# Optimization experiments

Hardware: AMD Instinct MI355X
Metric: run time of the kernel (lower is better)

The kernel has to match this reference:

```python
import jax, jax.numpy as jnp
import numpy as np

N, E, NF, EF = 2048, 65536, 128, 64
HID, NH, HD, FF, L = 256, 8, 32, 1024, 4
OUT, MAXN = 1280, 4096


def setup_inputs() -> dict:
    key = jax.random.key(0)
    ks = iter(jax.random.split(key, 64))
    def rn(shape, s=0.02):
        return jax.random.normal(next(ks), shape, jnp.float32) * s
    inp = dict(
        node_features=jax.random.normal(next(ks), (N, NF), jnp.float32),
        edge_features=jax.random.normal(next(ks), (E, EF), jnp.float32),
        edge_index=jax.random.randint(next(ks), (2, E), 0, N),
        W_node=rn((NF, HID)), b_node=jnp.zeros((HID,)),
        W_edge=rn((EF, HID)), b_edge=jnp.zeros((HID,)),
        pos_emb=rn((MAXN, HID), 1.0),
        Wq=rn((L, HID, HID)), bq=jnp.zeros((L, HID)),
        Wk=rn((L, HID, HID)), bk=jnp.zeros((L, HID)),
        Wv=rn((L, HID, HID)), bv=jnp.zeros((L, HID)),
        Wo=rn((L, HID, HID)), bo=jnp.zeros((L, HID)),
        Wep=rn((L, HID, NH)), bep=jnp.zeros((L, NH)),
        Wf1=rn((L, HID, FF)), bf1=jnp.zeros((L, FF)),
        Wf2=rn((L, FF, HID)), bf2=jnp.zeros((L, HID)),
        g1=jnp.ones((L, HID)), be1=jnp.zeros((L, HID)),
        g2=jnp.ones((L, HID)), be2=jnp.zeros((L, HID)),
        g_ln=jnp.ones((HID,)), b_ln=jnp.zeros((HID,)),
        Wp1=rn((HID, HID)), bp1=jnp.zeros((HID,)),
        Wp2=rn((HID, 1)), bp2=jnp.zeros((1,)),
        Wo1=rn((3 * HID, 2 * HID)), bo1=jnp.zeros((2 * HID,)),
        Wo2=rn((2 * HID, OUT)), bo2=jnp.zeros((OUT,)),
    )
    return inp


def _ln(x, g, b, eps=1e-5):
    m = x.mean(-1, keepdims=True)
    v = ((x - m) ** 2).mean(-1, keepdims=True)
    return (x - m) * jax.lax.rsqrt(v + eps) * g + b


def reference(node_features, edge_features, edge_index, W_node, b_node, W_edge,
              b_edge, pos_emb, Wq, bq, Wk, bk, Wv, bv, Wo, bo, Wep, bep,
              Wf1, bf1, Wf2, bf2, g1, be1, g2, be2, g_ln, b_ln,
              Wp1, bp1, Wp2, bp2, Wo1, bo1, Wo2, bo2):
    n = node_features.shape[0]
    src, dst = edge_index[0], edge_index[1]
    scale = float(np.sqrt(HD))
    # node encoding + learned positional embedding (n <= max_nodes path)
    x = node_features @ W_node + b_node + pos_emb[:n]
    edge_attr = edge_features @ W_edge + b_edge  # [E, HID]
    # symmetric adjacency mask with self-loops
    adj = jnp.zeros((n, n), bool).at[src, dst].set(True).at[dst, src].set(True)
    adj = adj.at[jnp.arange(n), jnp.arange(n)].set(True)
    for i in range(L):
        Q = (x @ Wq[i] + bq[i]).reshape(n, NH, HD)
        K = (x @ Wk[i] + bk[i]).reshape(n, NH, HD)
        V = (x @ Wv[i] + bv[i]).reshape(n, NH, HD)
        scores = jnp.einsum('nhd,mhd->nmh', Q, K) / scale  # [n, n, NH]
        ebias = edge_attr @ Wep[i] + bep[i]  # [E, NH]
        scores = scores.at[src, dst].add(ebias)  # accumulating scatter, same as per-edge loop
        scores = jnp.where(adj[:, None, :], scores.transpose(0, 2, 1), -jnp.inf)  # [n, NH, n]
        attn = jax.nn.softmax(scores, axis=-1)
        ctx = jnp.einsum('nhm,mhd->nhd', attn, V).reshape(n, HID)
        a = ctx @ Wo[i] + bo[i]
        x = _ln(x + a, g1[i], be1[i])
        f = jax.nn.gelu(x @ Wf1[i] + bf1[i], approximate=False) @ Wf2[i] + bf2[i]
        x = _ln(x + f, g2[i], be2[i])
    x = _ln(x, g_ln, b_ln)
    # global pooling (batch=None path): mean / max / attention
    mean_p = x.mean(0, keepdims=True)
    max_p = x.max(0, keepdims=True)
    aw = jax.nn.softmax(jnp.tanh(x @ Wp1 + bp1) @ Wp2 + bp2, axis=0)  # [n, 1]
    attn_p = (x * aw).sum(0, keepdims=True)
    g = jnp.concatenate([mean_p, max_p, attn_p], axis=1)  # [1, 3*HID]
    out = jax.nn.relu(g @ Wo1 + bo1) @ Wo2 + bo2  # [1, OUT]
    return out
```

## Files before the change

kernel.cpp:

```cpp
#include <hip/hip_runtime.h>
#include <math.h>

#define NNODE 2048
#define NEDGE 65536
#define HIDN  256
#define NHEAD 8
#define HDIM  32
#define FFD   1024
#define NLAYER 4
#define OUTD  1280
#define NNZ_MAX (2*NEDGE + NNODE)

typedef __attribute__((ext_vector_type(8))) short bf16x8;
typedef __attribute__((ext_vector_type(4))) float f32x4;

__device__ __forceinline__ unsigned short f2b(float f) {
    unsigned u = __float_as_uint(f);
    unsigned r = (u + 0x7fffu + ((u >> 16) & 1u)) >> 16;
    return (unsigned short)r;
}
__device__ __forceinline__ float b2f(unsigned short u) {
    return __uint_as_float((unsigned)u << 16);
}

template<int EPI, int OUT>
__global__ __launch_bounds__(256)
void mgemm(const unsigned short* __restrict__ A, const unsigned short* __restrict__ Bt,
           const float* __restrict__ bias, const float* __restrict__ extra,
           float* __restrict__ Cf, unsigned short* __restrict__ Cb,
           int M, int N, int K)
{
    __shared__ __align__(16) unsigned short As[64 * 40];
    __shared__ __align__(16) unsigned short Bs[64 * 40];
    int tid = threadIdx.x;
    int bm0 = blockIdx.y * 64, bn0 = blockIdx.x * 64;
    int wave = tid >> 6, lane = tid & 63;
    int wm = (wave >> 1) * 32, wn = (wave & 1) * 32;
    int srow = tid >> 2, skoff = (tid & 3) * 8;
    int lrow = lane & 15, quad = lane >> 4;
    f32x4 acc[2][2] = {};
    for (int k0 = 0; k0 < K; k0 += 32) {
        *(uint4*)(&As[srow*40 + skoff]) = *(const uint4*)(A  + (size_t)(bm0+srow)*K + k0 + skoff);
        *(uint4*)(&Bs[srow*40 + skoff]) = *(const uint4*)(Bt + (size_t)(bn0+srow)*K + k0 + skoff);
        __syncthreads();
        bf16x8 af[2], bfr[2];
        #pragma unroll
        for (int i = 0; i < 2; i++) af[i]  = *(const bf16x8*)(&As[(wm + i*16 + lrow)*40 + quad*8]);
        #pragma unroll
        for (int j = 0; j < 2; j++) bfr[j] = *(const bf16x8*)(&Bs[(wn + j*16 + lrow)*40 + quad*8]);
        #pragma unroll
        for (int i = 0; i < 2; i++)
            #pragma unroll
            for (int j = 0; j < 2; j++)
                acc[i][j] = __builtin_amdgcn_mfma_f32_16x16x32_bf16(af[i], bfr[j], acc[i][j], 0, 0, 0);
        __syncthreads();
    }
    #pragma unroll
    for (int i = 0; i < 2; i++)
        #pragma unroll
        for (int j = 0; j < 2; j++) {
            int col = bn0 + wn + j*16 + lrow;
            float bv = bias[col];
            #pragma unroll
            for (int r = 0; r < 4; r++) {
                int row = bm0 + wm + i*16 + quad*4 + r;
                float v = acc[i][j][r] + bv;
                if (EPI == 1) v = 0.5f * v * (1.f + erff(v * 0.70710678118654752f));
                else if (EPI == 2) v = tanhf(v);
                else if (EPI == 3) v += extra[(size_t)row*N + col];
                if (OUT == 0 || OUT == 2) Cf[(size_t)row*N + col] = v;
                if (OUT == 1 || OUT == 2) Cb[(size_t)row*N + col] = f2b(v);
            }
        }
}

__global__ __launch_bounds__(256)
void transpose_bf16(const float* __restrict__ src, unsigned short* __restrict__ dst,
                    int K, int N, long srcStride, long dstStride)
{
    __shared__ unsigned short tile[32][33];
    const float* s = src + (size_t)blockIdx.z * srcStride;
    unsigned short* d = dst + (size_t)blockIdx.z * dstStride;
    int n0 = blockIdx.x * 32, k0 = blockIdx.y * 32;
    int tx = threadIdx.x & 31, ty = threadIdx.x >> 5;
    #pragma unroll
    for (int i = 0; i < 4; i++)
        tile[ty + i*8][tx] = f2b(s[(size_t)(k0 + ty + i*8) * N + n0 + tx]);
    __syncthreads();
    #pragma unroll
    for (int i = 0; i < 4; i++)
        d[(size_t)(n0 + ty + i*8) * K + k0 + tx] = tile[tx][ty + i*8];
}

__global__ void conv_bf16(const float* __restrict__ s, unsigned short* __restrict__ d, int n)
{
    int t = blockIdx.x * 256 + threadIdx.x;
    if (t < n) d[t] = f2b(s[t]);
}

__global__ void concat_qkv_bias(const float* __restrict__ bq, const float* __restrict__ bk,
                                const float* __restrict__ bv, float* __restrict__ bqkv)
{
    int t = blockIdx.x * 256 + threadIdx.x;
    if (t >= NLAYER * 768) return;
    int l = t / 768, j = t % 768;
    float v = (j < 256) ? bq[l*256 + j] : (j < 512 ? bk[l*256 + j - 256] : bv[l*256 + j - 512]);
    bqkv[t] = v;
}

__global__ void adj_build(const int* __restrict__ src, const int* __restrict__ dst,
                          unsigned* __restrict__ adjbits)
{
    int t = blockIdx.x * blockDim.x + threadIdx.x;
    if (t < NEDGE) {
        int s = src[t], d = dst[t];
        atomicOr(&adjbits[(size_t)s*64 + (d >> 5)], 1u << (d & 31));
        atomicOr(&adjbits[(size_t)d*64 + (s >> 5)], 1u << (s & 31));
    }
    if (t < NNODE)
        atomicOr(&adjbits[(size_t)t*64 + (t >> 5)], 1u << (t & 31));
}

__global__ void row_rank(const unsigned* __restrict__ adjbits,
                         unsigned* __restrict__ rowcum, int* __restrict__ deg)
{
    int i = blockIdx.x * blockDim.x + threadIdx.x;
    if (i >= NNODE) return;
    unsigned c = 0;
    for (int w = 0; w < 64; w++) {
        rowcum[i*64 + w] = c;
        c += __popc(adjbits[i*64 + w]);
    }
    deg[i] = (int)c;
}

__global__ __launch_bounds__(256)
void scan_kernel(const int* __restrict__ deg, int* __restrict__ rowoff)
{
    __shared__ int part[256];
    int tid = threadIdx.x;
    int base = tid * 8;
    int local[8]; int s = 0;
    #pragma unroll
    for (int k = 0; k < 8; k++) { local[k] = s; s += deg[base + k]; }
    part[tid] = s;
    __syncthreads();
    for (int off = 1; off < 256; off <<= 1) {
        int v = (tid >= off) ? part[tid - off] : 0;
        __syncthreads();
        part[tid] += v;
        __syncthreads();
    }
    int pre = (tid == 0) ? 0 : part[tid - 1];
    #pragma unroll
    for (int k = 0; k < 8; k++) rowoff[base + k] = pre + local[k];
    if (tid == 255) rowoff[NNODE] = part[255];
}

__global__ void fill_cols(const unsigned* __restrict__ adjbits,
                          const int* __restrict__ rowoff, int* __restrict__ cols)
{
    int i = blockIdx.x * blockDim.x + threadIdx.x;
    if (i >= NNODE) return;
    int base = rowoff[i];
    for (int w = 0; w < 64; w++) {
        unsigned bits = adjbits[i*64 + w];
        while (bits) {
            int b = __ffs(bits) - 1;
            cols[base++] = w*32 + b;
            bits &= bits - 1;
        }
    }
}

__global__ void wcomb_kernel(const float* __restrict__ W_edge, const float* __restrict__ b_edge,
                             const float* __restrict__ Wep, const float* __restrict__ bep,
                             float* __restrict__ Wcomb, float* __restrict__ bcomb)
{
    int t = blockIdx.x * blockDim.x + threadIdx.x;
    if (t < 64*32) {
        int k = t >> 5, lh = t & 31, l = lh >> 3, h = lh & 7;
        float acc = 0.f;
        for (int c = 0; c < HIDN; c++)
            acc += W_edge[k*HIDN + c] * Wep[l*HIDN*NHEAD + c*NHEAD + h];
        Wcomb[k*32 + lh] = acc;
    } else if (t < 64*32 + 32) {
        int lh = t - 64*32, l = lh >> 3, h = lh & 7;
        float acc = bep[l*NHEAD + h];
        for (int c = 0; c < HIDN; c++)
            acc += b_edge[c] * Wep[l*HIDN*NHEAD + c*NHEAD + h];
        bcomb[lh] = acc;
    }
}

__global__ __launch_bounds__(256)
void ebias_kernel(const float* __restrict__ ef, const float* __restrict__ Wcomb,
                  const float* __restrict__ bcomb, float* __restrict__ out)
{
    __shared__ float Wl[64*32];
    __shared__ float bl[32];
    int tid = threadIdx.x;
    for (int k = tid; k < 64*32; k += 256) Wl[k] = Wcomb[k];
    if (tid < 32) bl[tid] = bcomb[tid];
    __syncthreads();
    int t = blockIdx.x * 256 + tid;
    int e = t >> 5, lh = t & 31;
    const float* f = ef + (size_t)e * 64;
    float acc = bl[lh];
    #pragma unroll
    for (int k = 0; k < 64; k++) acc += f[k] * Wl[k*32 + lh];
    out[(size_t)e*32 + lh] = acc;
}

__global__ void scatter_bias(const int* __restrict__ src, const int* __restrict__ dst,
                             const unsigned* __restrict__ adjbits,
                             const unsigned* __restrict__ rowcum,
                             const int* __restrict__ rowoff,
                             const float* __restrict__ ebias, float* __restrict__ bias_csr)
{
    int t = blockIdx.x * blockDim.x + threadIdx.x;
    int e = t >> 5;
    if (e >= NEDGE) return;
    int lh = t & 31;
    int s = src[e], d = dst[e];
    unsigned wbits = adjbits[(size_t)s*64 + (d >> 5)];
    int rank = (int)rowcum[(size_t)s*64 + (d >> 5)] + __popc(wbits & ((1u << (d & 31)) - 1u));
    int slot = rowoff[s] + rank;
    atomicAdd(&bias_csr[(size_t)slot*32 + lh], ebias[(size_t)e*32 + lh]);
}

__global__ __launch_bounds__(256)
void attn_kernel(const unsigned short* __restrict__ QKVb, const int* __restrict__ rowoff,
                 const int* __restrict__ cols, const float* __restrict__ bias_csr,
                 unsigned short* __restrict__ ctxb, int layer)
{
    __shared__ float mS[4][8], lS[4][8];
    __shared__ __align__(16) float accS[4][256];
    int i = blockIdx.x;
    int tid = threadIdx.x;
    int w = tid >> 6, lane = tid & 63;
    int h = lane >> 3;
    int off = lane * 4;
    ushort4 qu = *(const ushort4*)(QKVb + (size_t)i*768 + off);
    float4 qf = { b2f(qu.x), b2f(qu.y), b2f(qu.z), b2f(qu.w) };
    int start = rowoff[i], end = rowoff[i+1];
    int lh0 = layer * 8 + h;
    float m = -INFINITY, l = 0.f;
    float4 acc = {0.f, 0.f, 0.f, 0.f};
    for (int c0 = start + w; c0 < end; c0 += 256) {
        int myslot = c0 + 4*lane;
        int mycol = (myslot < end) ? cols[myslot] : 0;
        int lim = min(end, c0 + 256);
        int it = 0;
        for (int slot = c0; slot < lim; slot += 4, ++it) {
            int j = __shfl(mycol, it);
            ushort4 ku = *(const ushort4*)(QKVb + (size_t)j*768 + 256 + off);
            float s = qf.x*b2f(ku.x) + qf.y*b2f(ku.y) + qf.z*b2f(ku.z) + qf.w*b2f(ku.w);
            s += __shfl_xor(s, 1);
            s += __shfl_xor(s, 2);
            s += __shfl_xor(s, 4);
            s = s * 0.17677669529663687f + bias_csr[(size_t)slot*32 + lh0];
            float mn = fmaxf(m, s);
            float sc = __expf(m - mn);
            float p  = __expf(s - mn);
            ushort4 vu = *(const ushort4*)(QKVb + (size_t)j*768 + 512 + off);
            acc.x = acc.x*sc + p*b2f(vu.x);
            acc.y = acc.y*sc + p*b2f(vu.y);
            acc.z = acc.z*sc + p*b2f(vu.z);
            acc.w = acc.w*sc + p*b2f(vu.w);
            l = l*sc + p;
            m = mn;
        }
    }
    if ((lane & 7) == 0) { mS[w][h] = m; lS[w][h] = l; }
    *(float4*)&accS[w][off] = acc;
    __syncthreads();
    if (w == 0) {
        float m0 = mS[0][h], m1 = mS[1][h], m2 = mS[2][h], m3 = mS[3][h];
        float mx = fmaxf(fmaxf(m0, m1), fmaxf(m2, m3));
        float e0 = (m0 == -INFINITY) ? 0.f : __expf(m0 - mx);
        float e1 = (m1 == -INFINITY) ? 0.f : __expf(m1 - mx);
        float e2 = (m2 == -INFINITY) ? 0.f : __expf(m2 - mx);
        float e3 = (m3 == -INFINITY) ? 0.f : __expf(m3 - mx);
        float ls = lS[0][h]*e0 + lS[1][h]*e1 + lS[2][h]*e2 + lS[3][h]*e3;
        float4 a0 = *(float4*)&accS[0][off];
        float4 a1 = *(float4*)&accS[1][off];
        float4 a2 = *(float4*)&accS[2][off];
        float4 a3 = *(float4*)&accS[3][off];
        float inv = 1.f / ls;
        ushort4 o;
        o.x = f2b((a0.x*e0 + a1.x*e1 + a2.x*e2 + a3.x*e3) * inv);
        o.y = f2b((a0.y*e0 + a1.y*e1 + a2.y*e2 + a3.y*e3) * inv);
        o.z = f2b((a0.z*e0 + a1.z*e1 + a2.z*e2 + a3.z*e3) * inv);
        o.w = f2b((a0.w*e0 + a1.w*e1 + a2.w*e2 + a3.w*e3) * inv);
        *(ushort4*)(ctxb + (size_t)i*HIDN + off) = o;
    }
}

template<bool RES>
__global__ __launch_bounds__(256)
void ln_kernel(float* __restrict__ x, const float* __restrict__ r,
               const float* __restrict__ g, const float* __restrict__ b,
               unsigned short* __restrict__ xb)
{
    __shared__ float lds[4];
    int row = blockIdx.x, c = threadIdx.x;
    float v = x[(size_t)row*HIDN + c];
    if (RES) v += r[(size_t)row*HIDN + c];
    float s = v;
    for (int mm = 1; mm < 64; mm <<= 1) s += __shfl_xor(s, mm);
    if ((c & 63) == 0) lds[c >> 6] = s;
    __syncthreads();
    float mean = (lds[0] + lds[1] + lds[2] + lds[3]) * (1.f / HIDN);
    __syncthreads();
    float dv = v - mean;
    float qq = dv * dv;
    for (int mm = 1; mm < 64; mm <<= 1) qq += __shfl_xor(qq, mm);
    if ((c & 63) == 0) lds[c >> 6] = qq;
    __syncthreads();
    float var = (lds[0] + lds[1] + lds[2] + lds[3]) * (1.f / HIDN);
    float rs = rsqrtf(var + 1e-5f);
    float o = dv * rs * g[c] + b[c];
    x[(size_t)row*HIDN + c] = o;
    xb[(size_t)row*HIDN + c] = f2b(o);
}

__global__ void pool_score(const float* __restrict__ t, const float* __restrict__ Wp2,
                           const float* __restrict__ bp2, float* __restrict__ s)
{
    int i = blockIdx.x * blockDim.x + threadIdx.x;
    if (i >= NNODE) return;
    float acc = bp2[0];
    for (int c = 0; c < HIDN; c++) acc += t[(size_t)i*HIDN + c] * Wp2[c];
    s[i] = acc;
}

__global__ __launch_bounds__(1024)
void softmax_nodes(const float* __restrict__ s, float* __restrict__ aw)
{
    __shared__ float lds[16];
    __shared__ float red;
    int tid = threadIdx.x;
    float a = s[tid], b = s[tid + 1024];
    float mx = fmaxf(a, b);
    for (int mm = 1; mm < 64; mm <<= 1) mx = fmaxf(mx, __shfl_xor(mx, mm));
    if ((tid & 63) == 0) lds[tid >> 6] = mx;
    __syncthreads();
    if (tid == 0) { float v = -INFINITY; for (int k = 0; k < 16; k++) v = fmaxf(v, lds[k]); red = v; }
    __syncthreads();
    mx = red;
    float ea = __expf(a - mx), eb = __expf(b - mx);
    float ss = ea + eb;
    for (int mm = 1; mm < 64; mm <<= 1) ss += __shfl_xor(ss, mm);
    __syncthreads();
    if ((tid & 63) == 0) lds[tid >> 6] = ss;
    __syncthreads();
    if (tid == 0) { float v = 0.f; for (int k = 0; k < 16; k++) v += lds[k]; red = v; }
    __syncthreads();
    ss = red;
    aw[tid] = ea / ss;
    aw[tid + 1024] = eb / ss;
}

__global__ __launch_bounds__(256)
void pool_kernel(const float* __restrict__ x, const float* __restrict__ aw,
                 float* __restrict__ g)
{
    __shared__ float l1[4], l2[4], l3[4];
    int c = blockIdx.x, tid = threadIdx.x;
    float sm = 0.f, mx = -INFINITY, ap = 0.f;
    for (int r = tid; r < NNODE; r += 256) {
        float v = x[(size_t)r*HIDN + c];
        sm += v;
        mx = fmaxf(mx, v);
        ap += v * aw[r];
    }
    for (int mm = 1; mm < 64; mm <<= 1) {
        sm += __shfl_xor(sm, mm);
        mx = fmaxf(mx, __shfl_xor(mx, mm));
        ap += __shfl_xor(ap, mm);
    }
    if ((tid & 63) == 0) { int w = tid >> 6; l1[w] = sm; l2[w] = mx; l3[w] = ap; }
    __syncthreads();
    if (tid == 0) {
        sm = l1[0] + l1[1] + l1[2] + l1[3];
        mx = fmaxf(fmaxf(l2[0], l2[1]), fmaxf(l2[2], l2[3]));
        ap = l3[0] + l3[1] + l3[2] + l3[3];
        g[c]          = sm * (1.f / NNODE);
        g[HIDN + c]   = mx;
        g[2*HIDN + c] = ap;
    }
}

__global__ __launch_bounds__(512)
void head1(const float* __restrict__ g, const float* __restrict__ Wo1,
           const float* __restrict__ bo1, float* __restrict__ h1)
{
    __shared__ float gs[3*HIDN];
    int tid = threadIdx.x;
    for (int k = tid; k < 3*HIDN; k += 512) gs[k] = g[k];
    __syncthreads();
    float acc = bo1[tid];
    for (int k = 0; k < 3*HIDN; k++) acc += gs[k] * Wo1[(size_t)k*512 + tid];
    h1[tid] = fmaxf(acc, 0.f);
}

__global__ __launch_bounds__(256)
void head2(const float* __restrict__ h1, const float* __restrict__ Wo2,
           const float* __restrict__ bo2, float* __restrict__ out)
{
    __shared__ float hs[512];
    int tid = threadIdx.x;
    int j = blockIdx.x * 256 + tid;
    for (int k = tid; k < 512; k += 256) hs[k] = h1[k];
    __syncthreads();
    float acc = bo2[j];
    for (int k = 0; k < 512; k++) acc += hs[k] * Wo2[(size_t)k*OUTD + j];
    out[j] = acc;
}

extern "C" void kernel_launch(void* const* d_in, const int* in_sizes, int n_in,
                              void* d_out, int out_size, void* d_ws, size_t ws_size,
                              hipStream_t stream)
{
    const float* node_features = (const float*)d_in[0];
    const float* edge_features = (const float*)d_in[1];
    const int*   edge_index    = (const int*)d_in[2];
    const float* W_node = (const float*)d_in[3];
    const float* b_node = (const float*)d_in[4];
    const float* W_edge = (const float*)d_in[5];
    const float* b_edge = (const float*)d_in[6];
    const float* pos_emb = (const float*)d_in[7];
    const float* Wq = (const float*)d_in[8];
    const float* bq = (const float*)d_in[9];
    const float* Wk = (const float*)d_in[10];
    const float* bk = (const float*)d_in[11];
    const float* Wv = (const float*)d_in[12];
    const float* bv = (const float*)d_in[13];
    const float* Wo = (const float*)d_in[14];
    const float* bo = (const float*)d_in[15];
    const float* Wep = (const float*)d_in[16];
    const float* bep = (const float*)d_in[17];
    const float* Wf1 = (const float*)d_in[18];
    const float* bf1 = (const float*)d_in[19];
    const float* Wf2 = (const float*)d_in[20];
    const float* bf2 = (const float*)d_in[21];
    const float* g1  = (const float*)d_in[22];
    const float* be1 = (const float*)d_in[23];
    const float* g2  = (const float*)d_in[24];
    const float* be2 = (const float*)d_in[25];
    const float* g_ln = (const float*)d_in[26];
    const float* b_ln = (const float*)d_in[27];
    const float* Wp1 = (const float*)d_in[28];
    const float* bp1 = (const float*)d_in[29];
    const float* Wp2 = (const float*)d_in[30];
    const float* bp2 = (const float*)d_in[31];
    const float* Wo1 = (const float*)d_in[32];
    const float* bo1 = (const float*)d_in[33];
    const float* Wo2 = (const float*)d_in[34];
    const float* bo2 = (const float*)d_in[35];
    const int* src = edge_index;
    const int* dst = edge_index + NEDGE;

    char* w = (char*)d_ws;
    auto carve = [&](size_t nbytes) {
        void* p = (void*)w;
        w += (nbytes + 255) & ~(size_t)255;
        return p;
    };
    float* x        = (float*)carve((size_t)NNODE*HIDN*4);
    unsigned short* xb = (unsigned short*)carve((size_t)NNODE*HIDN*2);
    unsigned short* bufQKVb = (unsigned short*)carve((size_t)NNODE*768*2);
    float* bufO     = (float*)carve((size_t)NNODE*HIDN*4);
    float* bufP     = (float*)carve((size_t)NNODE*HIDN*4);
    unsigned short* bufAb = (unsigned short*)carve((size_t)NNODE*HIDN*2);
    void*  scratchA = carve((size_t)NEDGE*32*4);
    float* bufE     = (float*)scratchA;
    unsigned short* bufFb = (unsigned short*)scratchA;
    float* Wcomb    = (float*)carve(64*32*4);
    float* bcomb    = (float*)carve(32*4);
    unsigned* adjbits = (unsigned*)carve((size_t)NNODE*64*4);
    unsigned* rowcum  = (unsigned*)carve((size_t)NNODE*64*4);
    int* deg    = (int*)carve(NNODE*4);
    int* rowoff = (int*)carve((NNODE+1)*4);
    int* colsb  = (int*)carve((size_t)NNZ_MAX*4);
    float* bias_csr = (float*)carve((size_t)NNZ_MAX*32*4);
    float* sbuf  = (float*)carve(NNODE*4);
    float* awbuf = (float*)carve(NNODE*4);
    float* gbuf  = (float*)carve(3*HIDN*4);
    float* h1buf = (float*)carve(512*4);
    unsigned short* nf_b  = (unsigned short*)carve((size_t)NNODE*128*2);
    unsigned short* WnT   = (unsigned short*)carve((size_t)HIDN*128*2);
    unsigned short* WqkvT = (unsigned short*)carve((size_t)NLAYER*768*HIDN*2);
    float*          bqkv  = (float*)carve((size_t)NLAYER*768*4);
    unsigned short* WoT   = (unsigned short*)carve((size_t)NLAYER*HIDN*HIDN*2);
    unsigned short* Wf1T  = (unsigned short*)carve((size_t)NLAYER*FFD*HIDN*2);
    unsigned short* Wf2T  = (unsigned short*)carve((size_t)NLAYER*HIDN*FFD*2);
    unsigned short* Wp1T  = (unsigned short*)carve((size_t)HIDN*HIDN*2);

    hipMemsetAsync(adjbits, 0, (size_t)NNODE*64*4, stream);
    hipMemsetAsync(bias_csr, 0, (size_t)NNZ_MAX*32*4, stream);
    adj_build<<<(NEDGE+255)/256, 256, 0, stream>>>(src, dst, adjbits);
    row_rank<<<NNODE/256, 256, 0, stream>>>(adjbits, rowcum, deg);
    scan_kernel<<<1, 256, 0, stream>>>(deg, rowoff);
    fill_cols<<<NNODE/256, 256, 0, stream>>>(adjbits, rowoff, colsb);
    wcomb_kernel<<<(64*32+32+255)/256, 256, 0, stream>>>(W_edge, b_edge, Wep, bep, Wcomb, bcomb);
    ebias_kernel<<<(NEDGE*32)/256, 256, 0, stream>>>(edge_features, Wcomb, bcomb, bufE);
    scatter_bias<<<(NEDGE*32)/256, 256, 0, stream>>>(src, dst, adjbits, rowcum, rowoff, bufE, bias_csr);

    conv_bf16<<<(NNODE*128)/256, 256, 0, stream>>>(node_features, nf_b, NNODE*128);
    transpose_bf16<<<dim3(HIDN/32, 128/32, 1), 256, 0, stream>>>(W_node, WnT, 128, HIDN, 0, 0);
    transpose_bf16<<<dim3(8, 8, NLAYER), 256, 0, stream>>>(Wq, WqkvT,            HIDN, HIDN, 65536, 196608);
    transpose_bf16<<<dim3(8, 8, NLAYER), 256, 0, stream>>>(Wk, WqkvT + 65536,    HIDN, HIDN, 65536, 196608);
    transpose_bf16<<<dim3(8, 8, NLAYER), 256, 0, stream>>>(Wv, WqkvT + 131072,   HIDN, HIDN, 65536, 196608);
    transpose_bf16<<<dim3(8, 8, NLAYER), 256, 0, stream>>>(Wo, WoT, HIDN, HIDN, 65536, 65536);
    transpose_bf16<<<dim3(FFD/32, HIDN/32, NLAYER), 256, 0, stream>>>(Wf1, Wf1T, HIDN, FFD, 262144, 262144);
    transpose_bf16<<<dim3(HIDN/32, FFD/32, NLAYER), 256, 0, stream>>>(Wf2, Wf2T, FFD, HIDN, 262144, 262144);
    transpose_bf16<<<dim3(8, 8, 1), 256, 0, stream>>>(Wp1, Wp1T, HIDN, HIDN, 0, 0);
    concat_qkv_bias<<<(NLAYER*768+255)/256, 256, 0, stream>>>(bq, bk, bv, bqkv);

    mgemm<3,2><<<dim3(HIDN/64, NNODE/64), 256, 0, stream>>>(nf_b, WnT, b_node, pos_emb, x, xb, NNODE, HIDN, 128);

    for (int l = 0; l < NLAYER; l++) {
        mgemm<0,1><<<dim3(768/64, NNODE/64), 256, 0, stream>>>(
            xb, WqkvT + (size_t)l*768*HIDN, bqkv + l*768, nullptr, nullptr, bufQKVb, NNODE, 768, HIDN);
        attn_kernel<<<NNODE, 256, 0, stream>>>(bufQKVb, rowoff, colsb, bias_csr, bufAb, l);
        mgemm<0,0><<<dim3(HIDN/64, NNODE/64), 256, 0, stream>>>(
            bufAb, WoT + (size_t)l*HIDN*HIDN, bo + l*HIDN, nullptr, bufO, nullptr, NNODE, HIDN, HIDN);
        ln_kernel<true><<<NNODE, 256, 0, stream>>>(x, bufO, g1 + l*HIDN, be1 + l*HIDN, xb);
        mgemm<1,1><<<dim3(FFD/64, NNODE/64), 256, 0, stream>>>(
            xb, Wf1T + (size_t)l*FFD*HIDN, bf1 + l*FFD, nullptr, nullptr, bufFb, NNODE, FFD, HIDN);
        mgemm<0,0><<<dim3(HIDN/64, NNODE/64), 256, 0, stream>>>(
            bufFb, Wf2T + (size_t)l*HIDN*FFD, bf2 + l*HIDN, nullptr, bufO, nullptr, NNODE, HIDN, FFD);
        ln_kernel<true><<<NNODE, 256, 0, stream>>>(x, bufO, g2 + l*HIDN, be2 + l*HIDN, xb);
    }

    ln_kernel<false><<<NNODE, 256, 0, stream>>>(x, nullptr, g_ln, b_ln, xb);
    mgemm<2,0><<<dim3(HIDN/64, NNODE/64), 256, 0, stream>>>(xb, Wp1T, bp1, nullptr, bufP, nullptr, NNODE, HIDN, HIDN);
    pool_score<<<NNODE/256, 256, 0, stream>>>(bufP, Wp2, bp2, sbuf);
    softmax_nodes<<<1, 1024, 0, stream>>>(sbuf, awbuf);
    pool_kernel<<<HIDN, 256, 0, stream>>>(x, awbuf, gbuf);
    head1<<<1, 512, 0, stream>>>(gbuf, Wo1, bo1, h1buf);
    head2<<<OUTD/256, 256, 0, stream>>>(h1buf, Wo2, bo2, (float*)d_out);
}
```

Baseline: 554.9 us.

## Retile GEMM with large K chunks, fuse edge-bias scatter, parallelize fill_cols, merge launches

The GEMM now uses 32x64 output tiles and stages up to 256 K elements per shared-memory load, which cuts barriers and doubles the block count for the small-N GEMMs. The edge-bias projection is fused into the atomic scatter so the intermediate edge buffer is never written and read back. fill_cols becomes one thread per 32-bit word, using rowcum offsets, instead of one thread per row. The Q/K/V/O weight transposes are merged into a single launch, and the two memsets become one over adjacent buffers. The larger shared-memory footprint (about 50KB per block) may lower occupancy.

```diff
diff --git a/kernel.cpp b/kernel.cpp
--- a/kernel.cpp
+++ b/kernel.cpp
@@ -30,48 +30,53 @@
            float* __restrict__ Cf, unsigned short* __restrict__ Cb,
            int M, int N, int K)
 {
-    __shared__ __align__(16) unsigned short As[64 * 40];
-    __shared__ __align__(16) unsigned short Bs[64 * 40];
-    int tid = threadIdx.x;
-    int bm0 = blockIdx.y * 64, bn0 = blockIdx.x * 64;
+    __shared__ __align__(16) unsigned short As[32 * 264];
+    __shared__ __align__(16) unsigned short Bs[64 * 264];
+    int tid = threadIdx.x;
+    int bm0 = blockIdx.y * 32, bn0 = blockIdx.x * 64;
     int wave = tid >> 6, lane = tid & 63;
-    int wm = (wave >> 1) * 32, wn = (wave & 1) * 32;
-    int srow = tid >> 2, skoff = (tid & 3) * 8;
+    int wm = (wave & 1) * 16, wn = (wave >> 1) * 32;
     int lrow = lane & 15, quad = lane >> 4;
-    f32x4 acc[2][2] = {};
-    for (int k0 = 0; k0 < K; k0 += 32) {
-        *(uint4*)(&As[srow*40 + skoff]) = *(const uint4*)(A  + (size_t)(bm0+srow)*K + k0 + skoff);
-        *(uint4*)(&Bs[srow*40 + skoff]) = *(const uint4*)(Bt + (size_t)(bn0+srow)*K + k0 + skoff);
+    f32x4 acc[2] = {};
+    int kc = (K < 256) ? K : 256;
+    int ldl = kc + 8;
+    int upr = kc >> 3;
+    for (int k0 = 0; k0 < K; k0 += kc) {
+        int nA = 32 * upr;
+        for (int u = tid; u < nA; u += 256) {
+            int row = u / upr, col = (u % upr) * 8;
+            *(uint4*)(&As[row*ldl + col]) = *(const uint4*)(A + (size_t)(bm0+row)*K + k0 + col);
+        }
+        int nB = 64 * upr;
+        for (int u = tid; u < nB; u += 256) {
+            int row = u / upr, col = (u % upr) * 8;
+            *(uint4*)(&Bs[row*ldl + col]) = *(const uint4*)(Bt + (size_t)(bn0+row)*K + k0 + col);
+        }
         __syncthreads();
-        bf16x8 af[2], bfr[2];
+        for (int kk = 0; kk < kc; kk += 32) {
+            bf16x8 a  = *(const bf16x8*)(&As[(wm + lrow)*ldl + kk + quad*8]);
+            bf16x8 b0 = *(const bf16x8*)(&Bs[(wn + lrow)*ldl + kk + quad*8]);
+            bf16x8 b1 = *(const bf16x8*)(&Bs[(wn + 16 + lrow)*ldl + kk + quad*8]);
+            acc[0] = __builtin_amdgcn_mfma_f32_16x16x32_bf16(a, b0, acc[0], 0, 0, 0);
+            acc[1] = __builtin_amdgcn_mfma_f32_16x16x32_bf16(a, b1, acc[1], 0, 0, 0);
+        }
+        __syncthreads();
+    }
+    #pragma unroll
+    for (int j = 0; j < 2; j++) {
+        int col = bn0 + wn + j*16 + lrow;
+        float bv = bias[col];
         #pragma unroll
-        for (int i = 0; i < 2; i++) af[i]  = *(const bf16x8*)(&As[(wm + i*16 + lrow)*40 + quad*8]);
-        #pragma unroll
-        for (int j = 0; j < 2; j++) bfr[j] = *(const bf16x8*)(&Bs[(wn + j*16 + lrow)*40 + quad*8]);
-        #pragma unroll
-        for (int i = 0; i < 2; i++)
-            #pragma unroll
-            for (int j = 0; j < 2; j++)
-                acc[i][j] = __builtin_amdgcn_mfma_f32_16x16x32_bf16(af[i], bfr[j], acc[i][j], 0, 0, 0);
-        __syncthreads();
-    }
-    #pragma unroll
-    for (int i = 0; i < 2; i++)
-        #pragma unroll
-        for (int j = 0; j < 2; j++) {
-            int col = bn0 + wn + j*16 + lrow;
-            float bv = bias[col];
-            #pragma unroll
-            for (int r = 0; r < 4; r++) {
-                int row = bm0 + wm + i*16 + quad*4 + r;
-                float v = acc[i][j][r] + bv;
-                if (EPI == 1) v = 0.5f * v * (1.f + erff(v * 0.70710678118654752f));
-                else if (EPI == 2) v = tanhf(v);
-                else if (EPI == 3) v += extra[(size_t)row*N + col];
-                if (OUT == 0 || OUT == 2) Cf[(size_t)row*N + col] = v;
-                if (OUT == 1 || OUT == 2) Cb[(size_t)row*N + col] = f2b(v);
-            }
+        for (int r = 0; r < 4; r++) {
+            int row = bm0 + wm + quad*4 + r;
+            float v = acc[j][r] + bv;
+            if (EPI == 1) v = 0.5f * v * (1.f + erff(v * 0.70710678118654752f));
+            else if (EPI == 2) v = tanhf(v);
+            else if (EPI == 3) v += extra[(size_t)row*N + col];
+            if (OUT == 0 || OUT == 2) Cf[(size_t)row*N + col] = v;
+            if (OUT == 1 || OUT == 2) Cb[(size_t)row*N + col] = f2b(v);
         }
+    }
 }
 
 __global__ __launch_bounds__(256)
@@ -90,6 +95,28 @@
     #pragma unroll
     for (int i = 0; i < 4; i++)
         d[(size_t)(n0 + ty + i*8) * K + k0 + tx] = tile[tx][ty + i*8];
+}
+
+__global__ __launch_bounds__(256)
+void transpose_qkvo(const float* __restrict__ Wq, const float* __restrict__ Wk,
+                    const float* __restrict__ Wv, const float* __restrict__ Wo,
+                    unsigned short* __restrict__ WqkvT, unsigned short* __restrict__ WoT)
+{
+    __shared__ unsigned short tile[32][33];
+    int z = blockIdx.z;
+    int mat = z & 3, l = z >> 2;
+    const float* s = (mat == 0 ? Wq : mat == 1 ? Wk : mat == 2 ? Wv : Wo) + (size_t)l * 65536;
+    unsigned short* d = (mat < 3) ? WqkvT + (size_t)l*196608 + (size_t)mat*65536
+                                  : WoT + (size_t)l*65536;
+    int n0 = blockIdx.x * 32, k0 = blockIdx.y * 32;
+    int tx = threadIdx.x & 31, ty = threadIdx.x >> 5;
+    #pragma unroll
+    for (int i = 0; i < 4; i++)
+        tile[ty + i*8][tx] = f2b(s[(size_t)(k0 + ty + i*8) * 256 + n0 + tx]);
+    __syncthreads();
+    #pragma unroll
+    for (int i = 0; i < 4; i++)
+        d[(size_t)(n0 + ty + i*8) * 256 + k0 + tx] = tile[tx][ty + i*8];
 }
 
 __global__ void conv_bf16(const float* __restrict__ s, unsigned short* __restrict__ d, int n)
@@ -157,19 +184,18 @@
     if (tid == 255) rowoff[NNODE] = part[255];
 }
 
-__global__ void fill_cols(const unsigned* __restrict__ adjbits,
-                          const int* __restrict__ rowoff, int* __restrict__ cols)
-{
-    int i = blockIdx.x * blockDim.x + threadIdx.x;
-    if (i >= NNODE) return;
-    int base = rowoff[i];
-    for (int w = 0; w < 64; w++) {
-        unsigned bits = adjbits[i*64 + w];
-        while (bits) {
-            int b = __ffs(bits) - 1;
-            cols[base++] = w*32 + b;
-            bits &= bits - 1;
-        }
+__global__ __launch_bounds__(256)
+void fill_cols(const unsigned* __restrict__ adjbits, const int* __restrict__ rowoff,
+               const unsigned* __restrict__ rowcum, int* __restrict__ cols)
+{
+    int t = blockIdx.x * 256 + threadIdx.x;
+    int i = t >> 6, w = t & 63;
+    unsigned bits = adjbits[(size_t)i*64 + w];
+    int base = rowoff[i] + (int)rowcum[(size_t)i*64 + w];
+    while (bits) {
+        int b = __ffs(bits) - 1;
+        cols[base++] = w*32 + b;
+        bits &= bits - 1;
     }
 }
 
@@ -194,8 +220,12 @@
 }
 
 __global__ __launch_bounds__(256)
-void ebias_kernel(const float* __restrict__ ef, const float* __restrict__ Wcomb,
-                  const float* __restrict__ bcomb, float* __restrict__ out)
+void edge_bias_scatter(const float* __restrict__ ef, const float* __restrict__ Wcomb,
+                       const float* __restrict__ bcomb,
+                       const int* __restrict__ src, const int* __restrict__ dst,
+                       const unsigned* __restrict__ adjbits,
+                       const unsigned* __restrict__ rowcum,
+                       const int* __restrict__ rowoff, float* __restrict__ bias_csr)
 {
     __shared__ float Wl[64*32];
     __shared__ float bl[32];
@@ -209,24 +239,11 @@
     float acc = bl[lh];
     #pragma unroll
     for (int k = 0; k < 64; k++) acc += f[k] * Wl[k*32 + lh];
-    out[(size_t)e*32 + lh] = acc;
-}
-
-__global__ void scatter_bias(const int* __restrict__ src, const int* __restrict__ dst,
-                             const unsigned* __restrict__ adjbits,
-                             const unsigned* __restrict__ rowcum,
-                             const int* __restrict__ rowoff,
-                             const float* __restrict__ ebias, float* __restrict__ bias_csr)
-{
-    int t = blockIdx.x * blockDim.x + threadIdx.x;
-    int e = t >> 5;
-    if (e >= NEDGE) return;
-    int lh = t & 31;
     int s = src[e], d = dst[e];
     unsigned wbits = adjbits[(size_t)s*64 + (d >> 5)];
     int rank = (int)rowcum[(size_t)s*64 + (d >> 5)] + __popc(wbits & ((1u << (d & 31)) - 1u));
     int slot = rowoff[s] + rank;
-    atomicAdd(&bias_csr[(size_t)slot*32 + lh], ebias[(size_t)e*32 + lh]);
+    atomicAdd(&bias_csr[(size_t)slot*32 + lh], acc);
 }
 
 __global__ __launch_bounds__(256)
@@ -474,17 +491,15 @@
     float* bufO     = (float*)carve((size_t)NNODE*HIDN*4);
     float* bufP     = (float*)carve((size_t)NNODE*HIDN*4);
     unsigned short* bufAb = (unsigned short*)carve((size_t)NNODE*HIDN*2);
-    void*  scratchA = carve((size_t)NEDGE*32*4);
-    float* bufE     = (float*)scratchA;
-    unsigned short* bufFb = (unsigned short*)scratchA;
+    unsigned short* bufFb = (unsigned short*)carve((size_t)NNODE*FFD*2);
     float* Wcomb    = (float*)carve(64*32*4);
     float* bcomb    = (float*)carve(32*4);
     unsigned* adjbits = (unsigned*)carve((size_t)NNODE*64*4);
+    float* bias_csr = (float*)carve((size_t)NNZ_MAX*32*4);
     unsigned* rowcum  = (unsigned*)carve((size_t)NNODE*64*4);
     int* deg    = (int*)carve(NNODE*4);
     int* rowoff = (int*)carve((NNODE+1)*4);
     int* colsb  = (int*)carve((size_t)NNZ_MAX*4);
-    float* bias_csr = (float*)carve((size_t)NNZ_MAX*32*4);
     float* sbuf  = (float*)carve(NNODE*4);
     float* awbuf = (float*)carve(NNODE*4);
     float* gbuf  = (float*)carve(3*HIDN*4);
@@ -498,45 +513,41 @@
     unsigned short* Wf2T  = (unsigned short*)carve((size_t)NLAYER*HIDN*FFD*2);
     unsigned short* Wp1T  = (unsigned short*)carve((size_t)HIDN*HIDN*2);
 
-    hipMemsetAsync(adjbits, 0, (size_t)NNODE*64*4, stream);
-    hipMemsetAsync(bias_csr, 0, (size_t)NNZ_MAX*32*4, stream);
+    hipMemsetAsync(adjbits, 0, (size_t)NNODE*64*4 + (size_t)NNZ_MAX*32*4, stream);
     adj_build<<<(NEDGE+255)/256, 256, 0, stream>>>(src, dst, adjbits);
     row_rank<<<NNODE/256, 256, 0, stream>>>(adjbits, rowcum, deg);
     scan_kernel<<<1, 256, 0, stream>>>(deg, rowoff);
-    fill_cols<<<NNODE/256, 256, 0, stream>>>(adjbits, rowoff, colsb);
+    fill_cols<<<(NNODE*64)/256, 256, 0, stream>>>(adjbits, rowoff, rowcum, colsb);
     wcomb_kernel<<<(64*32+32+255)/256, 256, 0, stream>>>(W_edge, b_edge, Wep, bep, Wcomb, bcomb);
-    ebias_kernel<<<(NEDGE*32)/256, 256, 0, stream>>>(edge_features, Wcomb, bcomb, bufE);
-    scatter_bias<<<(NEDGE*32)/256, 256, 0, stream>>>(src, dst, adjbits, rowcum, rowoff, bufE, bias_csr);
+    edge_bias_scatter<<<(NEDGE*32)/256, 256, 0, stream>>>(
+        edge_features, Wcomb, bcomb, src, dst, adjbits, rowcum, rowoff, bias_csr);
 
     conv_bf16<<<(NNODE*128)/256, 256, 0, stream>>>(node_features, nf_b, NNODE*128);
-    transpose_bf16<<<dim3(HIDN/32, 128/32, 1), 256, 0, stream>>>(W_node, WnT, 128, HIDN, 0, 0);
-    transpose_bf16<<<dim3(8, 8, NLAYER), 256, 0, stream>>>(Wq, WqkvT,            HIDN, HIDN, 65536, 196608);
-    transpose_bf16<<<dim3(8, 8, NLAYER), 256, 0, stream>>>(Wk, WqkvT + 65536,    HIDN, HIDN, 65536, 196608);
-    transpose_bf16<<<dim3(8, 8, NLAYER), 256, 0, stream>>>(Wv, WqkvT + 131072,   HIDN, HIDN, 65536, 196608);
-    transpose_bf16<<<dim3(8, 8, NLAYER), 256, 0, stream>>>(Wo, WoT, HIDN, HIDN, 65536, 65536);
+    transpose_qkvo<<<dim3(8, 8, 16), 256, 0, stream>>>(Wq, Wk, Wv, Wo, WqkvT, WoT);
     transpose_bf16<<<dim3(FFD/32, HIDN/32, NLAYER), 256, 0, stream>>>(Wf1, Wf1T, HIDN, FFD, 262144, 262144);
     transpose_bf16<<<dim3(HIDN/32, FFD/32, NLAYER), 256, 0, stream>>>(Wf2, Wf2T, FFD, HIDN, 262144, 262144);
+    transpose_bf16<<<dim3(HIDN/32, 128/32, 1), 256, 0, stream>>>(W_node, WnT, 128, HIDN, 0, 0);
     transpose_bf16<<<dim3(8, 8, 1), 256, 0, stream>>>(Wp1, Wp1T, HIDN, HIDN, 0, 0);
     concat_qkv_bias<<<(NLAYER*768+255)/256, 256, 0, stream>>>(bq, bk, bv, bqkv);
 
-    mgemm<3,2><<<dim3(HIDN/64, NNODE/64), 256, 0, stream>>>(nf_b, WnT, b_node, pos_emb, x, xb, NNODE, HIDN, 128);
+    mgemm<3,2><<<dim3(HIDN/64, NNODE/32), 256, 0, stream>>>(nf_b, WnT, b_node, pos_emb, x, xb, NNODE, HIDN, 128);
 
     for (int l = 0; l < NLAYER; l++) {
-        mgemm<0,1><<<dim3(768/64, NNODE/64), 256, 0, stream>>>(
+        mgemm<0,1><<<dim3(768/64, NNODE/32), 256, 0, stream>>>(
             xb, WqkvT + (size_t)l*768*HIDN, bqkv + l*768, nullptr, nullptr, bufQKVb, NNODE, 768, HIDN);
         attn_kernel<<<NNODE, 256, 0, stream>>>(bufQKVb, rowoff, colsb, bias_csr, bufAb, l);
-        mgemm<0,0><<<dim3(HIDN/64, NNODE/64), 256, 0, stream>>>(
+        mgemm<0,0><<<dim3(HIDN/64, NNODE/32), 256, 0, stream>>>(
             bufAb, WoT + (size_t)l*HIDN*HIDN, bo + l*HIDN, nullptr, bufO, nullptr, NNODE, HIDN, HIDN);
         ln_kernel<true><<<NNODE, 256, 0, stream>>>(x, bufO, g1 + l*HIDN, be1 + l*HIDN, xb);
-        mgemm<1,1><<<dim3(FFD/64, NNODE/64), 256, 0, stream>>>(
+        mgemm<1,1><<<dim3(FFD/64, NNODE/32), 256, 0, stream>>>(
             xb, Wf1T + (size_t)l*FFD*HIDN, bf1 + l*FFD, nullptr, nullptr, bufFb, NNODE, FFD, HIDN);
-        mgemm<0,0><<<dim3(HIDN/64, NNODE/64), 256, 0, stream>>>(
+        mgemm<0,0><<<dim3(HIDN/64, NNODE/32), 256, 0, stream>>>(
             bufFb, Wf2T + (size_t)l*HIDN*FFD, bf2 + l*HIDN, nullptr, bufO, nullptr, NNODE, HIDN, FFD);
         ln_kernel<true><<<NNODE, 256, 0, stream>>>(x, bufO, g2 + l*HIDN, be2 + l*HIDN, xb);
     }
 
     ln_kernel<false><<<NNODE, 256, 0, stream>>>(x, nullptr, g_ln, b_ln, xb);
-    mgemm<2,0><<<dim3(HIDN/64, NNODE/64), 256, 0, stream>>>(xb, Wp1T, bp1, nullptr, bufP, nullptr, NNODE, HIDN, HIDN);
+    mgemm<2,0><<<dim3(HIDN/64, NNODE/32), 256, 0, stream>>>(xb, Wp1T, bp1, nullptr, bufP, nullptr, NNODE, HIDN, HIDN);
     pool_score<<<NNODE/256, 256, 0, stream>>>(bufP, Wp2, bp2, sbuf);
     softmax_nodes<<<1, 1024, 0, stream>>>(sbuf, awbuf);
     pool_kernel<<<HIDN, 256, 0, stream>>>(x, awbuf, gbuf);
```

Measured after the change: 575.9 us. +3.8%, slower.
